# Optimization experiments

Measured on AMD Instinct MI355X. Metric: run time of the kernel, lower is better.

Reference implementation:

```python
import jax, jax.numpy as jnp
import numpy as np

B, S, D, E, K = 4, 4096, 2048, 64, 2

def setup_inputs() -> dict:
    key = jax.random.key(0)
    kx, kw = jax.random.split(key)
    x = jax.random.normal(kx, (B, S, D), dtype=jnp.float32)
    W = jax.random.normal(kw, (E, D), dtype=jnp.float32) * (1.0 / np.sqrt(D))
    b = jnp.zeros((E,), dtype=jnp.float32)
    return {"x": x, "W": W, "b": b, "k": K}

def reference(x, W, b, k):
    # logits: [B, S, E]
    logits = jnp.einsum('bsd,ed->bse', x, W) + b
    probs = jax.nn.softmax(logits, axis=-1)
    topk_probs, topk_experts = jax.lax.top_k(probs, k)  # [B,S,k]
    # one-hot over experts, OR-reduce over k -> bool mask [B,S,E]
    onehot = jax.nn.one_hot(topk_experts, E, dtype=jnp.int32)  # [B,S,k,E]
    masks = onehot.sum(axis=-2).astype(jnp.bool_)
    return (masks, probs)
```

## Files before the change

kernel.cpp:

```cpp
#include <hip/hip_runtime.h>
#include <math.h>

#define NTOK    16384
#define DDIM    2048
#define NEXP    64
#define PSTRIDE (NTOK * NEXP)

#define AS1 __attribute__((address_space(1)))
#define AS3 __attribute__((address_space(3)))

typedef _Float16 half8   __attribute__((ext_vector_type(8)));
typedef float    floatx4 __attribute__((ext_vector_type(4)));

__global__ __launch_bounds__(256) void wconv_kernel(
    const float* __restrict__ W, _Float16* __restrict__ ws)
{
    const int g  = blockIdx.x * 256 + threadIdx.x;
    const int s  = g >> 10;
    const int c  = g & 1023;
    const int q  = c & 3;
    const int e  = (c >> 2) & 63;
    const int pl = (c >> 8) & 1;
    const int kk = (c >> 9) & 1;
    const int k  = s * 64 + kk * 32 + q * 8;

    const float* src = &W[(size_t)e * DDIM + k];
    floatx4 w0 = *(const floatx4*)src;
    floatx4 w1 = *(const floatx4*)(src + 4);

    half8 o;
#pragma unroll
    for (int i = 0; i < 4; ++i) {
        float f0 = w0[i], f1 = w1[i];
        _Float16 h0 = (_Float16)f0, h1 = (_Float16)f1;
        if (pl == 0) { o[i] = h0; o[4 + i] = h1; }
        else {
            o[i]     = (_Float16)((f0 - (float)h0) * 2048.0f);
            o[4 + i] = (_Float16)((f1 - (float)h1) * 2048.0f);
        }
    }
    *(half8*)(ws + (size_t)g * 8) = o;
}

__global__ __launch_bounds__(512, 2) void gemm_partial(
    const float* __restrict__ x,
    const _Float16* __restrict__ ws,
    float* __restrict__ part)
{
    __shared__ __align__(16) char lds[2][16384];

    const int tid  = threadIdx.x;
    const int lane = tid & 63;
    const int wid  = tid >> 6;
    const int bm   = blockIdx.x >> 2;
    const int ks   = blockIdx.x & 3;
    const int T0   = bm * 256;
    const int mrow = lane & 15;
    const int quad = lane >> 4;

    floatx4 acc_hh[2][4], acc_md[2][4];
#pragma unroll
    for (int m = 0; m < 2; ++m)
#pragma unroll
        for (int j = 0; j < 4; ++j) { acc_hh[m][j] = (floatx4)0.0f; acc_md[m][j] = (floatx4)0.0f; }

    const float* xbase = x + (size_t)(T0 + wid * 32 + mrow) * DDIM + ks * 512 + quad * 8;
    const char* wsrc = (const char*)ws + (size_t)(ks * 8) * 16384 + (size_t)lane * 16;

#define DMA(P, B)                                                              \
    {                                                                          \
        const char* gs = wsrc + (size_t)(P) * 16384;                           \
        __builtin_amdgcn_global_load_lds(                                      \
            (const AS1 unsigned int*)(const void*)(gs + wid * 1024),           \
            (AS3 unsigned int*)(void*)&lds[B][wid * 1024], 16, 0, 0);          \
        __builtin_amdgcn_global_load_lds(                                      \
            (const AS1 unsigned int*)(const void*)(gs + 8192 + wid * 1024),    \
            (AS3 unsigned int*)(void*)&lds[B][8192 + wid * 1024], 16, 0, 0);   \
    }

#define XLOAD(P, DST)                                                          \
    {                                                                          \
        _Pragma("unroll")                                                      \
        for (int m_ = 0; m_ < 2; ++m_)                                         \
        _Pragma("unroll")                                                      \
        for (int kk_ = 0; kk_ < 2; ++kk_)                                      \
        _Pragma("unroll")                                                      \
        for (int hf_ = 0; hf_ < 2; ++hf_)                                      \
            (DST)[m_ * 4 + kk_ * 2 + hf_] = *(const floatx4*)(                 \
                xbase + (size_t)m_ * 16 * DDIM + (P) * 64 + kk_ * 32 + hf_ * 4); \
    }

    floatx4 xc[8], xn[8];

    XLOAD(0, xc);
    DMA(0, 0);
    __syncthreads();

    for (int p = 0; p < 8; ++p) {
        if (p < 7) {
            XLOAD(p + 1, xn);
            DMA(p + 1, (p + 1) & 1);
        }

        const _Float16* lb = (const _Float16*)lds[p & 1];
#pragma unroll
        for (int kk = 0; kk < 2; ++kk) {
            half8 bh[4], bl[4];
#pragma unroll
            for (int j = 0; j < 4; ++j) {
                const int e = j * 16 + mrow;
                bh[j] = *(const half8*)(lb + ((kk * 2 + 0) * 64 + e) * 32 + quad * 8);
                bl[j] = *(const half8*)(lb + ((kk * 2 + 1) * 64 + e) * 32 + quad * 8);
            }
#pragma unroll
            for (int m = 0; m < 2; ++m) {
                half8 a_hi, a_lo;
                floatx4 v0 = xc[m * 4 + kk * 2];
                floatx4 v1 = xc[m * 4 + kk * 2 + 1];
#pragma unroll
                for (int q = 0; q < 4; ++q) {
                    float fv = v0[q];
                    _Float16 hh = (_Float16)fv;
                    a_hi[q] = hh;
                    a_lo[q] = (_Float16)((fv - (float)hh) * 2048.0f);
                }
#pragma unroll
                for (int q = 0; q < 4; ++q) {
                    float fv = v1[q];
                    _Float16 hh = (_Float16)fv;
                    a_hi[4 + q] = hh;
                    a_lo[4 + q] = (_Float16)((fv - (float)hh) * 2048.0f);
                }
#pragma unroll
                for (int j = 0; j < 4; ++j) {
                    acc_hh[m][j] = __builtin_amdgcn_mfma_f32_16x16x32_f16(a_hi, bh[j], acc_hh[m][j], 0, 0, 0);
                    acc_md[m][j] = __builtin_amdgcn_mfma_f32_16x16x32_f16(a_hi, bl[j], acc_md[m][j], 0, 0, 0);
                    acc_md[m][j] = __builtin_amdgcn_mfma_f32_16x16x32_f16(a_lo, bh[j], acc_md[m][j], 0, 0, 0);
                }
            }
        }

        if (p < 7) {
#pragma unroll
            for (int i = 0; i < 8; ++i) xc[i] = xn[i];
        }
        __syncthreads();
    }

    float* pw = part + ((size_t)(ks * 64 + bm)) * 16384 + wid * 2048 + lane;
#pragma unroll
    for (int m = 0; m < 2; ++m)
#pragma unroll
        for (int j = 0; j < 4; ++j)
#pragma unroll
            for (int r = 0; r < 4; ++r)
                pw[m * 1024 + (j * 4 + r) * 64] =
                    acc_hh[m][j][r] + acc_md[m][j][r] * (1.0f / 2048.0f);
}

__global__ __launch_bounds__(256) void reduce_epilogue(
    const float* __restrict__ part,
    const float* __restrict__ bias,
    float* __restrict__ out)
{
    const int tid  = threadIdx.x;
    const int lane = tid & 63;
    const int u    = blockIdx.x * 4 + (tid >> 6);
    const int bm   = u >> 4;
    const int w8   = (u >> 1) & 7;
    const int m    = u & 1;
    const int mrow = lane & 15;
    const int quad = lane >> 4;
    const int tb   = bm * 256 + w8 * 32 + m * 16;

    const float* pb = part + (size_t)bm * 16384 + w8 * 2048 + m * 1024 + lane;

    float lg[4][4];
#pragma unroll
    for (int j = 0; j < 4; ++j) {
        const float bj = bias[j * 16 + mrow];
#pragma unroll
        for (int r = 0; r < 4; ++r) {
            const int f = j * 4 + r;
            float s0 = pb[(size_t)0 * 1048576 + f * 64];
            float s1 = pb[(size_t)1 * 1048576 + f * 64];
            float s2 = pb[(size_t)2 * 1048576 + f * 64];
            float s3 = pb[(size_t)3 * 1048576 + f * 64];
            lg[j][r] = (s0 + s1) + (s2 + s3) + bj;
        }
    }

    const int c = mrow;
#pragma unroll
    for (int r = 0; r < 4; ++r) {
        const int trow = tb + quad * 4 + r;

        float mx = lg[0][r];
#pragma unroll
        for (int j = 1; j < 4; ++j) mx = fmaxf(mx, lg[j][r]);
#pragma unroll
        for (int off = 1; off <= 8; off <<= 1) mx = fmaxf(mx, __shfl_xor(mx, off));

        float pj[4], s = 0.0f;
#pragma unroll
        for (int j = 0; j < 4; ++j) { pj[j] = __expf(lg[j][r] - mx); s += pj[j]; }
#pragma unroll
        for (int off = 1; off <= 8; off <<= 1) s += __shfl_xor(s, off);
        const float rinv = 1.0f / s;

        float v1 = -1e30f, v2 = -1e30f; int i1 = -1, i2 = -1;
#pragma unroll
        for (int j = 0; j < 4; ++j) {
            float v = lg[j][r]; int e = j * 16 + c;
            if (v > v1 || (v == v1 && e < i1)) { v2 = v1; i2 = i1; v1 = v; i1 = e; }
            else if (v > v2 || (v == v2 && e < i2)) { v2 = v; i2 = e; }
        }
#pragma unroll
        for (int off = 1; off <= 8; off <<= 1) {
            float u1 = __shfl_xor(v1, off); int q1 = __shfl_xor(i1, off);
            float u2 = __shfl_xor(v2, off); int q2 = __shfl_xor(i2, off);
            if (u1 > v1 || (u1 == v1 && q1 < i1)) {
                if (v1 > u2 || (v1 == u2 && i1 < q2)) { v2 = v1; i2 = i1; }
                else                                   { v2 = u2; i2 = q2; }
                v1 = u1; i1 = q1;
            } else {
                if (u1 > v2 || (u1 == v2 && q1 < i2)) { v2 = u1; i2 = q1; }
            }
        }

#pragma unroll
        for (int j = 0; j < 4; ++j) {
            const int col = j * 16 + c;
            const size_t o = (size_t)trow * NEXP + col;
            out[o]           = (col == i1 || col == i2) ? 1.0f : 0.0f;
            out[PSTRIDE + o] = pj[j] * rinv;
        }
    }
}

extern "C" void kernel_launch(void* const* d_in, const int* in_sizes, int n_in,
                              void* d_out, int out_size, void* d_ws, size_t ws_size,
                              hipStream_t stream) {
    const float* x = (const float*)d_in[0];
    const float* W = (const float*)d_in[1];
    const float* b = (const float*)d_in[2];
    (void)in_sizes; (void)n_in; (void)out_size; (void)ws_size;
    float* out = (float*)d_out;

    _Float16* ws  = (_Float16*)d_ws;
    float*    prt = (float*)((char*)d_ws + (1 << 19));

    hipLaunchKernelGGL(wconv_kernel,    dim3(128), dim3(256), 0, stream, W, ws);
    hipLaunchKernelGGL(gemm_partial,    dim3(256), dim3(512), 0, stream, x, ws, prt);
    hipLaunchKernelGGL(reduce_epilogue, dim3(256), dim3(256), 0, stream, prt, b, out);
}
```

Measured before the change: 209.6 us.

## Load whole K-slice of weights into LDS once with swizzle and register prefetch

The GEMM kernel now DMAs the block's entire 128KB weight slice into LDS once at the start, replacing the per-step double-buffered DMA. This removes all per-iteration __syncthreads barriers. The weight layout is XOR-swizzled in the conversion kernel to avoid LDS bank conflicts. The main loop now runs over 16 steps of K=32, with a 2-deep register prefetch of x and a 1-deep prefetch of the B fragments. The cost is much larger LDS use per block (128KB), which likely drops occupancy from 2 blocks per CU to 1. Register pressure also rises.

```diff
diff --git a/kernel.cpp b/kernel.cpp
--- a/kernel.cpp
+++ b/kernel.cpp
@@ -16,13 +16,14 @@
     const float* __restrict__ W, _Float16* __restrict__ ws)
 {
     const int g  = blockIdx.x * 256 + threadIdx.x;
-    const int s  = g >> 10;
-    const int c  = g & 1023;
-    const int q  = c & 3;
-    const int e  = (c >> 2) & 63;
-    const int pl = (c >> 8) & 1;
-    const int kk = (c >> 9) & 1;
-    const int k  = s * 64 + kk * 32 + q * 8;
+    const int ks = g >> 13;
+    const int L  = g & 8191;
+    const int s  = L >> 9;
+    const int pl = (L >> 8) & 1;
+    const int e  = (L >> 2) & 63;
+    const int qp = L & 3;
+    const int q  = qp ^ ((e >> 1) & 3);
+    const int k  = ks * 512 + s * 32 + q * 8;
 
     const float* src = &W[(size_t)e * DDIM + k];
     floatx4 w0 = *(const floatx4*)src;
@@ -47,104 +48,105 @@
     const _Float16* __restrict__ ws,
     float* __restrict__ part)
 {
-    __shared__ __align__(16) char lds[2][16384];
+    __shared__ __align__(16) _Float16 blds[65536];
 
     const int tid  = threadIdx.x;
     const int lane = tid & 63;
     const int wid  = tid >> 6;
     const int bm   = blockIdx.x >> 2;
     const int ks   = blockIdx.x & 3;
-    const int T0   = bm * 256;
     const int mrow = lane & 15;
     const int quad = lane >> 4;
 
+    {
+        const char* gs = (const char*)ws + (size_t)ks * 131072 + (size_t)tid * 16;
+        char*       ld = (char*)blds + tid * 16;
+#pragma unroll
+        for (int i = 0; i < 16; ++i)
+            __builtin_amdgcn_global_load_lds(
+                (const AS1 unsigned int*)(const void*)(gs + i * 8192),
+                (AS3 unsigned int*)(void*)(ld + i * 8192), 16, 0, 0);
+    }
+
+    const float* xbase = x + (size_t)(bm * 256 + wid * 32 + mrow) * DDIM + ks * 512 + quad * 8;
+
+    int ebase[4];
+#pragma unroll
+    for (int j = 0; j < 4; ++j) {
+        const int e = j * 16 + mrow;
+        ebase[j] = e * 32 + ((quad ^ ((e >> 1) & 3)) << 3);
+    }
+
     floatx4 acc_hh[2][4], acc_md[2][4];
 #pragma unroll
     for (int m = 0; m < 2; ++m)
 #pragma unroll
         for (int j = 0; j < 4; ++j) { acc_hh[m][j] = (floatx4)0.0f; acc_md[m][j] = (floatx4)0.0f; }
 
-    const float* xbase = x + (size_t)(T0 + wid * 32 + mrow) * DDIM + ks * 512 + quad * 8;
-    const char* wsrc = (const char*)ws + (size_t)(ks * 8) * 16384 + (size_t)lane * 16;
-
-#define DMA(P, B)                                                              \
-    {                                                                          \
-        const char* gs = wsrc + (size_t)(P) * 16384;                           \
-        __builtin_amdgcn_global_load_lds(                                      \
-            (const AS1 unsigned int*)(const void*)(gs + wid * 1024),           \
-            (AS3 unsigned int*)(void*)&lds[B][wid * 1024], 16, 0, 0);          \
-        __builtin_amdgcn_global_load_lds(                                      \
-            (const AS1 unsigned int*)(const void*)(gs + 8192 + wid * 1024),    \
-            (AS3 unsigned int*)(void*)&lds[B][8192 + wid * 1024], 16, 0, 0);   \
-    }
-
-#define XLOAD(P, DST)                                                          \
+#define XL(S, D)                                                               \
     {                                                                          \
         _Pragma("unroll")                                                      \
-        for (int m_ = 0; m_ < 2; ++m_)                                         \
-        _Pragma("unroll")                                                      \
-        for (int kk_ = 0; kk_ < 2; ++kk_)                                      \
-        _Pragma("unroll")                                                      \
-        for (int hf_ = 0; hf_ < 2; ++hf_)                                      \
-            (DST)[m_ * 4 + kk_ * 2 + hf_] = *(const floatx4*)(                 \
-                xbase + (size_t)m_ * 16 * DDIM + (P) * 64 + kk_ * 32 + hf_ * 4); \
-    }
-
-    floatx4 xc[8], xn[8];
-
-    XLOAD(0, xc);
-    DMA(0, 0);
+        for (int m_ = 0; m_ < 2; ++m_) {                                       \
+            (D)[m_ * 2]     = *(const floatx4*)(xbase + (size_t)m_ * 16 * DDIM + (S) * 32); \
+            (D)[m_ * 2 + 1] = *(const floatx4*)(xbase + (size_t)m_ * 16 * DDIM + (S) * 32 + 4); \
+        }                                                                      \
+    }
+
+    floatx4 x0[4], x1[4], x2[4];
+    XL(0, x0);
+    XL(1, x1);
+
     __syncthreads();
 
-    for (int p = 0; p < 8; ++p) {
-        if (p < 7) {
-            XLOAD(p + 1, xn);
-            DMA(p + 1, (p + 1) & 1);
-        }
-
-        const _Float16* lb = (const _Float16*)lds[p & 1];
-#pragma unroll
-        for (int kk = 0; kk < 2; ++kk) {
-            half8 bh[4], bl[4];
+    half8 cbh[4], cbl[4], nbh[4], nbl[4];
+#pragma unroll
+    for (int j = 0; j < 4; ++j) {
+        cbh[j] = *(const half8*)(blds + ebase[j]);
+        cbl[j] = *(const half8*)(blds + 2048 + ebase[j]);
+    }
+
+#pragma unroll 2
+    for (int s = 0; s < 16; ++s) {
+        if (s + 2 < 16) XL(s + 2, x2);
+        if (s + 1 < 16) {
+            const _Float16* bp = blds + (s + 1) * 4096;
 #pragma unroll
             for (int j = 0; j < 4; ++j) {
-                const int e = j * 16 + mrow;
-                bh[j] = *(const half8*)(lb + ((kk * 2 + 0) * 64 + e) * 32 + quad * 8);
-                bl[j] = *(const half8*)(lb + ((kk * 2 + 1) * 64 + e) * 32 + quad * 8);
-            }
-#pragma unroll
-            for (int m = 0; m < 2; ++m) {
-                half8 a_hi, a_lo;
-                floatx4 v0 = xc[m * 4 + kk * 2];
-                floatx4 v1 = xc[m * 4 + kk * 2 + 1];
-#pragma unroll
-                for (int q = 0; q < 4; ++q) {
-                    float fv = v0[q];
-                    _Float16 hh = (_Float16)fv;
-                    a_hi[q] = hh;
-                    a_lo[q] = (_Float16)((fv - (float)hh) * 2048.0f);
-                }
-#pragma unroll
-                for (int q = 0; q < 4; ++q) {
-                    float fv = v1[q];
-                    _Float16 hh = (_Float16)fv;
-                    a_hi[4 + q] = hh;
-                    a_lo[4 + q] = (_Float16)((fv - (float)hh) * 2048.0f);
-                }
-#pragma unroll
-                for (int j = 0; j < 4; ++j) {
-                    acc_hh[m][j] = __builtin_amdgcn_mfma_f32_16x16x32_f16(a_hi, bh[j], acc_hh[m][j], 0, 0, 0);
-                    acc_md[m][j] = __builtin_amdgcn_mfma_f32_16x16x32_f16(a_hi, bl[j], acc_md[m][j], 0, 0, 0);
-                    acc_md[m][j] = __builtin_amdgcn_mfma_f32_16x16x32_f16(a_lo, bh[j], acc_md[m][j], 0, 0, 0);
-                }
-            }
-        }
-
-        if (p < 7) {
-#pragma unroll
-            for (int i = 0; i < 8; ++i) xc[i] = xn[i];
-        }
-        __syncthreads();
+                nbh[j] = *(const half8*)(bp + ebase[j]);
+                nbl[j] = *(const half8*)(bp + 2048 + ebase[j]);
+            }
+        }
+
+#pragma unroll
+        for (int m = 0; m < 2; ++m) {
+            half8 a_hi, a_lo;
+            floatx4 v0 = x0[m * 2], v1 = x0[m * 2 + 1];
+#pragma unroll
+            for (int q = 0; q < 4; ++q) {
+                float fv = v0[q];
+                _Float16 hh = (_Float16)fv;
+                a_hi[q] = hh;
+                a_lo[q] = (_Float16)((fv - (float)hh) * 2048.0f);
+            }
+#pragma unroll
+            for (int q = 0; q < 4; ++q) {
+                float fv = v1[q];
+                _Float16 hh = (_Float16)fv;
+                a_hi[4 + q] = hh;
+                a_lo[4 + q] = (_Float16)((fv - (float)hh) * 2048.0f);
+            }
+#pragma unroll
+            for (int j = 0; j < 4; ++j) {
+                acc_hh[m][j] = __builtin_amdgcn_mfma_f32_16x16x32_f16(a_hi, cbh[j], acc_hh[m][j], 0, 0, 0);
+                acc_md[m][j] = __builtin_amdgcn_mfma_f32_16x16x32_f16(a_hi, cbl[j], acc_md[m][j], 0, 0, 0);
+                acc_md[m][j] = __builtin_amdgcn_mfma_f32_16x16x32_f16(a_lo, cbh[j], acc_md[m][j], 0, 0, 0);
+            }
+        }
+
+#pragma unroll
+        for (int i = 0; i < 4; ++i) { x0[i] = x1[i]; x1[i] = x2[i]; }
+#pragma unroll
+        for (int j = 0; j < 4; ++j) { cbh[j] = nbh[j]; cbl[j] = nbl[j]; }
     }
 
     float* pw = part + ((size_t)(ks * 64 + bm)) * 16384 + wid * 2048 + lane;
```

Result: no change. 213.6 us (+1.9%).
